# Performance work log

Measured on AMD Instinct MI355X. Metric: run time of the kernel, lower is better.

## Reference

```python
import jax, jax.numpy as jnp
import numpy as np

LN_EPS = 1e-6

def layernorm(x, scale, bias):
    mu = jnp.mean(x, axis=-1, keepdims=True)
    var = jnp.mean(jnp.square(x - mu), axis=-1, keepdims=True)
    return (x - mu) * jax.lax.rsqrt(var + LN_EPS) * scale + bias

def setup_inputs() -> dict:
    key = jax.random.key(0)
    ks = jax.random.split(key, 8)
    B, S, Dm = 2, 2048, 1024
    H, Dh, E, De = 16, 64, 8, 1024
    s = 0.02
    return {
        'x': jax.random.normal(ks[0], (B, S, Dm), jnp.float32),
        'ln1_scale': jnp.ones((Dm,), jnp.float32),
        'ln1_bias': jnp.zeros((Dm,), jnp.float32),
        'Wqkv': jax.random.normal(ks[1], (Dm, 3 * H * Dh), jnp.float32) * s,
        'bqkv': jnp.zeros((3 * H * Dh,), jnp.float32),
        'Wo': jax.random.normal(ks[2], (H * Dh, Dm), jnp.float32) * s,
        'bo': jnp.zeros((Dm,), jnp.float32),
        'ln2_scale': jnp.ones((Dm,), jnp.float32),
        'ln2_bias': jnp.zeros((Dm,), jnp.float32),
        'router_W': jax.random.normal(ks[3], (Dm, E), jnp.float32) * s,
        'We': jax.random.normal(ks[4], (E, Dm, De), jnp.float32) * s,
        'be': jnp.zeros((E, De), jnp.float32),
        'Wmo': jax.random.normal(ks[5], (De, Dm), jnp.float32) * s,
        'bmo': jnp.zeros((Dm,), jnp.float32),
    }

def reference(x, ln1_scale, ln1_bias, Wqkv, bqkv, Wo, bo,
              ln2_scale, ln2_bias, router_W, We, be, Wmo, bmo):
    B, S, Dm = x.shape
    H, Dh = 16, 64
    # ---- attention sublayer ----
    y = layernorm(x, ln1_scale, ln1_bias)
    qkv = (y @ Wqkv + bqkv).reshape(B, S, 3, H, Dh)
    qkv = jnp.transpose(qkv, (2, 0, 3, 1, 4))  # [3,B,H,S,Dh]
    q, k, v = qkv[0], qkv[1], qkv[2]
    scale = 1.0 / jnp.sqrt(jnp.float32(Dh))
    attn = jax.nn.softmax(jnp.einsum('bhsd,bhtd->bhst', q, k) * scale, axis=-1)
    o = jnp.einsum('bhst,bhtd->bhsd', attn, v)
    o = jnp.transpose(o, (0, 2, 1, 3)).reshape(B, S, H * Dh)
    x = x + (o @ Wo + bo)
    # ---- dense soft-MoE sublayer ----
    y = layernorm(x, ln2_scale, ln2_bias)
    routing = jax.nn.softmax(jnp.einsum('bsh,he->bse', y, router_W), axis=-1)
    expert_out = jnp.einsum('bsh,ehf->bsef', y, We) + be  # [B,S,E,De]
    combined = jnp.einsum('bse,bsef->bsf', routing, expert_out)
    x = x + (combined @ Wmo + bmo)
    return x
```

## Files before the change

kernel.cpp:

```cpp
#include <hip/hip_runtime.h>
#include <hip/hip_bf16.h>

typedef unsigned short u16;
typedef float f32x4 __attribute__((ext_vector_type(4)));
typedef short s16x8 __attribute__((ext_vector_type(8)));
typedef unsigned short u16x4 __attribute__((ext_vector_type(4)));
typedef unsigned short u16x8 __attribute__((ext_vector_type(8)));

#define T_TOK 4096
#define DM 1024
#define NQKV 3072
#define LN_EPS 1e-6f
#define KDIM 1024
#define NT 32

__device__ __forceinline__ void gll16(const void* g, void* l) {
    __builtin_amdgcn_global_load_lds(
        (const __attribute__((address_space(1))) void*)g,
        (__attribute__((address_space(3))) void*)l, 16, 0, 0);
}

__device__ __forceinline__ void xcd_swz(int& bx, int& by) {
    const int gx = gridDim.x, gy = gridDim.y;
    const int nwg = gx * gy;
    const int lin = by * gx + bx;
    const int cpx = nwg >> 3;
    const int swz = (lin & 7) * cpx + (lin >> 3);
    bx = swz % gx;
    by = swz / gx;
}

__device__ __forceinline__ void bf16_split(float x, u16& hi, u16& lo) {
    unsigned xb = __float_as_uint(x);
    unsigned rh = xb + 0x7fffu + ((xb >> 16) & 1u);
    hi = (u16)(rh >> 16);
    float hf = __uint_as_float(((unsigned)hi) << 16);
    float rs = x - hf;
    unsigned rb = __float_as_uint(rs);
    unsigned rl = rb + 0x7fffu + ((rb >> 16) & 1u);
    lo = (u16)(rl >> 16);
}
__device__ __forceinline__ u16 f2bf(float x) {
    unsigned xb = __float_as_uint(x);
    return (u16)((xb + 0x7fffu + ((xb >> 16) & 1u)) >> 16);
}
__device__ __forceinline__ float bf16_comb(u16 h, u16 l) {
    return __uint_as_float(((unsigned)h) << 16) + __uint_as_float(((unsigned)l) << 16);
}

#define MFMA3(ACC, AH, AL, BH, BL) { \
    ACC = __builtin_amdgcn_mfma_f32_16x16x32_bf16(AH, BH, ACC, 0, 0, 0); \
    ACC = __builtin_amdgcn_mfma_f32_16x16x32_bf16(AH, BL, ACC, 0, 0, 0); \
    ACC = __builtin_amdgcn_mfma_f32_16x16x32_bf16(AL, BH, ACC, 0, 0, 0); }

__global__ __launch_bounds__(256)
void convert_w(const float* __restrict__ src, u16* __restrict__ dh,
               u16* __restrict__ dl, int K, int N) {
    const int e = blockIdx.z;
    src += (size_t)e * K * N;
    dh  += (size_t)e * K * N;
    dl  += (size_t)e * K * N;
    __shared__ float ts[64][65];
    const int t = threadIdx.x;
    const int k0 = blockIdx.y * 64, n0 = blockIdx.x * 64;
    const int r = t >> 4, c4 = (t & 15) * 4;
    #pragma unroll
    for (int i = 0; i < 4; ++i) {
        const int kr = r + i * 16;
        float4 v = *(const float4*)(src + (size_t)(k0 + kr) * N + n0 + c4);
        ts[kr][c4 + 0] = v.x; ts[kr][c4 + 1] = v.y;
        ts[kr][c4 + 2] = v.z; ts[kr][c4 + 3] = v.w;
    }
    __syncthreads();
    #pragma unroll
    for (int i = 0; i < 4; ++i) {
        const int nr = r + i * 16;
        u16x4 h4, l4;
        #pragma unroll
        for (int j = 0; j < 4; ++j) {
            u16 h, l; bf16_split(ts[c4 + j][nr], h, l);
            h4[j] = h; l4[j] = l;
        }
        *(u16x4*)(dh + (size_t)(n0 + nr) * K + k0 + c4) = h4;
        *(u16x4*)(dl + (size_t)(n0 + nr) * K + k0 + c4) = l4;
    }
}

__global__ __launch_bounds__(256)
void ln_kernel(const float* __restrict__ x, const float* __restrict__ sc,
               const float* __restrict__ bi, u16* __restrict__ yh,
               u16* __restrict__ yl) {
    const int row = blockIdx.x;
    const int t = threadIdx.x;
    const float* xr = x + (size_t)row * DM;
    float4 v = *(const float4*)(xr + t * 4);
    float s  = v.x + v.y + v.z + v.w;
    float s2 = v.x*v.x + v.y*v.y + v.z*v.z + v.w*v.w;
    #pragma unroll
    for (int off = 32; off; off >>= 1) {
        s  += __shfl_down(s, off);
        s2 += __shfl_down(s2, off);
    }
    __shared__ float ss[4], ss2[4];
    const int wid = t >> 6;
    if ((t & 63) == 0) { ss[wid] = s; ss2[wid] = s2; }
    __syncthreads();
    const float tot  = ss[0] + ss[1] + ss[2] + ss[3];
    const float tot2 = ss2[0] + ss2[1] + ss2[2] + ss2[3];
    const float mu  = tot * (1.0f / DM);
    const float var = tot2 * (1.0f / DM) - mu * mu;
    const float rcp = rsqrtf(var + LN_EPS);
    float4 sv = *(const float4*)(sc + t * 4);
    float4 bv = *(const float4*)(bi + t * 4);
    float o[4];
    o[0] = (v.x - mu) * rcp * sv.x + bv.x;
    o[1] = (v.y - mu) * rcp * sv.y + bv.y;
    o[2] = (v.z - mu) * rcp * sv.z + bv.z;
    o[3] = (v.w - mu) * rcp * sv.w + bv.w;
    u16x4 h4, l4;
    #pragma unroll
    for (int j = 0; j < 4; ++j) { u16 h, l; bf16_split(o[j], h, l); h4[j] = h; l4[j] = l; }
    *(u16x4*)(yh + (size_t)row * DM + t * 4) = h4;
    *(u16x4*)(yl + (size_t)row * DM + t * 4) = l4;
}

__global__ __launch_bounds__(256, 2)
void qkv_gemm(const u16* __restrict__ Ah, const u16* __restrict__ Al,
              const u16* __restrict__ Bh, const u16* __restrict__ Bl,
              const float* __restrict__ bias,
              u16* __restrict__ qh, u16* __restrict__ ql,
              u16* __restrict__ kh, u16* __restrict__ kl,
              u16* __restrict__ vh, u16* __restrict__ vl) {
    __shared__ __align__(16) u16 Ahs[128 * 32], Als[128 * 32];
    __shared__ __align__(16) u16 Bhs[128 * 32], Bls[128 * 32];
    int bx = blockIdx.x, by = blockIdx.y;
    xcd_swz(bx, by);
    const int t = threadIdx.x;
    const int m0 = by * 128, n0 = bx * 128;
    const int lane = t & 63, wid = t >> 6;
    const int wm = wid >> 1, wn = wid & 1;
    const int lr = lane & 15, lc = lane >> 4;
    const int srow = lane >> 2, skk = (lane & 3) * 8;
    const int w32 = wid * 32;
    const u16* Agh = Ah + (size_t)(m0 + w32 + srow) * KDIM + skk;
    const u16* Agl = Al + (size_t)(m0 + w32 + srow) * KDIM + skk;
    const u16* Bgh = Bh + (size_t)(n0 + w32 + srow) * KDIM + skk;
    const u16* Bgl = Bl + (size_t)(n0 + w32 + srow) * KDIM + skk;

    f32x4 acc[4][4];
    #pragma unroll
    for (int i = 0; i < 4; ++i)
        #pragma unroll
        for (int j = 0; j < 4; ++j)
            #pragma unroll
            for (int r = 0; r < 4; ++r) acc[i][j][r] = 0.0f;

    for (int kt = 0; kt < NT; ++kt) {
        const int ko = kt * 32;
        gll16(Agh + ko,              &Ahs[w32 * 32]);
        gll16(Agh + ko + 16 * KDIM,  &Ahs[(w32 + 16) * 32]);
        gll16(Agl + ko,              &Als[w32 * 32]);
        gll16(Agl + ko + 16 * KDIM,  &Als[(w32 + 16) * 32]);
        gll16(Bgh + ko,              &Bhs[w32 * 32]);
        gll16(Bgh + ko + 16 * KDIM,  &Bhs[(w32 + 16) * 32]);
        gll16(Bgl + ko,              &Bls[w32 * 32]);
        gll16(Bgl + ko + 16 * KDIM,  &Bls[(w32 + 16) * 32]);
        __syncthreads();
        s16x8 fa_h[4], fa_l[4], fb_h[4], fb_l[4];
        #pragma unroll
        for (int fi = 0; fi < 4; ++fi) {
            const int ro = (wm * 64 + fi * 16 + lr) * 32 + lc * 8;
            fa_h[fi] = *(const s16x8*)&Ahs[ro];
            fa_l[fi] = *(const s16x8*)&Als[ro];
        }
        #pragma unroll
        for (int fj = 0; fj < 4; ++fj) {
            const int ro = (wn * 64 + fj * 16 + lr) * 32 + lc * 8;
            fb_h[fj] = *(const s16x8*)&Bhs[ro];
            fb_l[fj] = *(const s16x8*)&Bls[ro];
        }
        #pragma unroll
        for (int fi = 0; fi < 4; ++fi)
            #pragma unroll
            for (int fj = 0; fj < 4; ++fj)
                MFMA3(acc[fi][fj], fa_h[fi], fa_l[fi], fb_h[fj], fb_l[fj])
        __syncthreads();
    }

    #pragma unroll
    for (int fj = 0; fj < 4; ++fj) {
        const int col = n0 + wn * 64 + fj * 16 + lr;
        const int sec = col >> 10;
        const int hh = (col & 1023) >> 6;
        const int dd = col & 63;
        const float bv = bias[col];
        u16* ph = (sec == 0) ? qh : (sec == 1) ? kh : vh;
        u16* pl = (sec == 0) ? ql : (sec == 1) ? kl : vl;
        #pragma unroll
        for (int fi = 0; fi < 4; ++fi)
            #pragma unroll
            for (int r = 0; r < 4; ++r) {
                const int row = m0 + wm * 64 + fi * 16 + lc * 4 + r;
                const int b = row >> 11, s = row & 2047;
                const size_t idx = ((size_t)(b * 16 + hh) * 2048 + s) * 64 + dd;
                u16 h, l; bf16_split(acc[fi][fj][r] + bv, h, l);
                ph[idx] = h; pl[idx] = l;
            }
    }
}

template<int MODE>
__global__ __launch_bounds__(256, 2)
void gemm_mfma(const u16* __restrict__ Ah, const u16* __restrict__ Al,
               const u16* __restrict__ Bh, const u16* __restrict__ Bl,
               const float* __restrict__ bias, const float* __restrict__ res,
               float* __restrict__ C, u16* __restrict__ Cb, int N) {
    __shared__ __align__(16) u16 Ahs[128 * 32], Als[128 * 32];
    __shared__ __align__(16) u16 Bhs[128 * 32], Bls[128 * 32];
    int bx = blockIdx.x, by = blockIdx.y;
    xcd_swz(bx, by);
    const int t = threadIdx.x;
    const int m0 = by * 128, n0 = bx * 128;
    const int lane = t & 63, wid = t >> 6;
    const int wm = wid >> 1, wn = wid & 1;
    const int lr = lane & 15, lc = lane >> 4;
    const int srow = lane >> 2, skk = (lane & 3) * 8;
    const int w32 = wid * 32;
    const u16* Agh = Ah + (size_t)(m0 + w32 + srow) * KDIM + skk;
    const u16* Agl = Al + (size_t)(m0 + w32 + srow) * KDIM + skk;
    const u16* Bgh = Bh + (size_t)(n0 + w32 + srow) * KDIM + skk;
    const u16* Bgl = Bl + (size_t)(n0 + w32 + srow) * KDIM + skk;

    f32x4 acc[4][4];
    #pragma unroll
    for (int i = 0; i < 4; ++i)
        #pragma unroll
        for (int j = 0; j < 4; ++j)
            #pragma unroll
            for (int r = 0; r < 4; ++r) acc[i][j][r] = 0.0f;

    for (int kt = 0; kt < NT; ++kt) {
        const int ko = kt * 32;
        gll16(Agh + ko,              &Ahs[w32 * 32]);
        gll16(Agh + ko + 16 * KDIM,  &Ahs[(w32 + 16) * 32]);
        gll16(Agl + ko,              &Als[w32 * 32]);
        gll16(Agl + ko + 16 * KDIM,  &Als[(w32 + 16) * 32]);
        gll16(Bgh + ko,              &Bhs[w32 * 32]);
        gll16(Bgh + ko + 16 * KDIM,  &Bhs[(w32 + 16) * 32]);
        gll16(Bgl + ko,              &Bls[w32 * 32]);
        gll16(Bgl + ko + 16 * KDIM,  &Bls[(w32 + 16) * 32]);
        __syncthreads();
        s16x8 fa_h[4], fa_l[4], fb_h[4], fb_l[4];
        #pragma unroll
        for (int fi = 0; fi < 4; ++fi) {
            const int ro = (wm * 64 + fi * 16 + lr) * 32 + lc * 8;
            fa_h[fi] = *(const s16x8*)&Ahs[ro];
            fa_l[fi] = *(const s16x8*)&Als[ro];
        }
        #pragma unroll
        for (int fj = 0; fj < 4; ++fj) {
            const int ro = (wn * 64 + fj * 16 + lr) * 32 + lc * 8;
            fb_h[fj] = *(const s16x8*)&Bhs[ro];
            fb_l[fj] = *(const s16x8*)&Bls[ro];
        }
        #pragma unroll
        for (int fi = 0; fi < 4; ++fi)
            #pragma unroll
            for (int fj = 0; fj < 4; ++fj)
                MFMA3(acc[fi][fj], fa_h[fi], fa_l[fi], fb_h[fj], fb_l[fj])
        __syncthreads();
    }

    #pragma unroll
    for (int fj = 0; fj < 4; ++fj) {
        const int col = n0 + wn * 64 + fj * 16 + lr;
        const float bv = bias[col];
        #pragma unroll
        for (int fi = 0; fi < 4; ++fi)
            #pragma unroll
            for (int r = 0; r < 4; ++r) {
                const int row = m0 + wm * 64 + fi * 16 + lc * 4 + r;
                if (MODE == 0) {
                    C[(size_t)row * N + col] =
                        acc[fi][fj][r] + bv + res[(size_t)row * N + col];
                } else {
                    Cb[(size_t)row * N + col] = f2bf(acc[fi][fj][r] + bv);
                }
            }
    }
}

__global__ __launch_bounds__(256)
void combine_kernel(const u16* __restrict__ eo, const float* __restrict__ r,
                    u16* __restrict__ ch, u16* __restrict__ cl) {
    const int t = blockIdx.x;
    const int f0 = threadIdx.x * 4;
    const float* rt = r + (size_t)t * 8;
    float rr[8];
    #pragma unroll
    for (int e = 0; e < 8; ++e) rr[e] = rt[e];
    const u16* row = eo + (size_t)t * 8192;
    float acc[4] = {0.0f, 0.0f, 0.0f, 0.0f};
    #pragma unroll
    for (int e = 0; e < 8; ++e) {
        u16x4 v = *(const u16x4*)(row + e * 1024 + f0);
        #pragma unroll
        for (int j = 0; j < 4; ++j)
            acc[j] += rr[e] * __uint_as_float(((unsigned)v[j]) << 16);
    }
    u16x4 h4, l4;
    #pragma unroll
    for (int j = 0; j < 4; ++j) { u16 h, l; bf16_split(acc[j], h, l); h4[j] = h; l4[j] = l; }
    *(u16x4*)(ch + (size_t)t * 1024 + f0) = h4;
    *(u16x4*)(cl + (size_t)t * 1024 + f0) = l4;
}

#define VTS 72
__global__ __launch_bounds__(256, 3)
void attn_kernel(const u16* __restrict__ qh, const u16* __restrict__ ql,
                 const u16* __restrict__ kh, const u16* __restrict__ kl,
                 const u16* __restrict__ vh, const u16* __restrict__ vl,
                 u16* __restrict__ oh, u16* __restrict__ ol) {
    __shared__ __align__(16) u16 Khs[64 * 64], Kls[64 * 64];
    __shared__ __align__(16) u16 Vth[64 * VTS], Vtl[64 * VTS];
    __shared__ __align__(16) u16 Phs[4 * 16 * VTS], Pls[4 * 16 * VTS];
    const int t = threadIdx.x;
    const int lane = t & 63, w = t >> 6;
    const int lr = lane & 15, lc = lane >> 4;
    const int q0 = blockIdx.x * 64;
    const int bh = blockIdx.y;
    const int b = bh >> 4, h = bh & 15;
    const size_t head = (size_t)bh * 2048 * 64;

    s16x8 qf_h[2], qf_l[2];
    {
        const size_t qrow = head + (size_t)(q0 + w * 16 + lr) * 64;
        #pragma unroll
        for (int c = 0; c < 2; ++c) {
            qf_h[c] = *(const s16x8*)(qh + qrow + c * 32 + lc * 8);
            qf_l[c] = *(const s16x8*)(ql + qrow + c * 32 + lc * 8);
        }
    }

    f32x4 o4[4];
    #pragma unroll
    for (int dt = 0; dt < 4; ++dt)
        #pragma unroll
        for (int r = 0; r < 4; ++r) o4[dt][r] = 0.0f;
    float m_run[4], l_run[4];
    #pragma unroll
    for (int r = 0; r < 4; ++r) { m_run[r] = -3.0e38f; l_run[r] = 0.0f; }

    char* const kbase_h = (char*)Khs;
    char* const kbase_l = (char*)Kls;
    u16* const pmy_h = Phs + w * 16 * VTS;
    u16* const pmy_l = Pls + w * 16 * VTS;

    const int dbase = (w & 1) * 32;
    const u16* kplane = (w >> 1) ? kl : kh;
    const u16* vplane = (w >> 1) ? vl : vh;
    char* const kdst = (w >> 1) ? kbase_l : kbase_h;
    u16* const vdst = (w >> 1) ? Vtl : Vth;

    u16x8 kreg[4], vreg[4];
    {
        const size_t grow = head + (size_t)(0 * 64 + lane) * 64 + dbase;
        #pragma unroll
        for (int jj = 0; jj < 4; ++jj) {
            kreg[jj] = *(const u16x8*)(kplane + grow + jj * 8);
            vreg[jj] = *(const u16x8*)(vplane + grow + jj * 8);
        }
    }

    for (int kt = 0; kt < 32; ++kt) {
        __syncthreads();
        #pragma unroll
        for (int jj = 0; jj < 4; ++jj) {
            const int off = (lane * 128 + dbase * 2 + jj * 16) ^ ((lane & 7) << 4);
            *(u16x8*)(kdst + off) = kreg[jj];
            #pragma unroll
            for (int i = 0; i < 8; ++i)
                vdst[(dbase + jj * 8 + i) * VTS + lane] = vreg[jj][i];
        }
        if (kt + 1 < 32) {
            const size_t grow = head + (size_t)((kt + 1) * 64 + lane) * 64 + dbase;
            #pragma unroll
            for (int jj = 0; jj < 4; ++jj) {
                kreg[jj] = *(const u16x8*)(kplane + grow + jj * 8);
                vreg[jj] = *(const u16x8*)(vplane + grow + jj * 8);
            }
        }
        __syncthreads();

        f32x4 s4[4];
        const int kxor = (lr & 7) << 4;
        #pragma unroll
        for (int j = 0; j < 4; ++j) {
            #pragma unroll
            for (int r = 0; r < 4; ++r) s4[j][r] = 0.0f;
            #pragma unroll
            for (int c = 0; c < 2; ++c) {
                const int off = ((j * 16 + lr) * 128 + c * 64 + lc * 16) ^ kxor;
                s16x8 kb_h = *(const s16x8*)(kbase_h + off);
                s16x8 kb_l = *(const s16x8*)(kbase_l + off);
                MFMA3(s4[j], qf_h[c], qf_l[c], kb_h, kb_l)
            }
        }
        #pragma unroll
        for (int j = 0; j < 4; ++j)
            #pragma unroll
            for (int r = 0; r < 4; ++r) s4[j][r] *= 0.125f;
        #pragma unroll
        for (int r = 0; r < 4; ++r) {
            float tm = fmaxf(fmaxf(s4[0][r], s4[1][r]), fmaxf(s4[2][r], s4[3][r]));
            tm = fmaxf(tm, __shfl_xor(tm, 1));
            tm = fmaxf(tm, __shfl_xor(tm, 2));
            tm = fmaxf(tm, __shfl_xor(tm, 4));
            tm = fmaxf(tm, __shfl_xor(tm, 8));
            const float mn = fmaxf(m_run[r], tm);
            const float corr = __expf(m_run[r] - mn);
            m_run[r] = mn;
            float ps = 0.0f;
            #pragma unroll
            for (int j = 0; j < 4; ++j) {
                const float p = __expf(s4[j][r] - mn);
                s4[j][r] = p;
                ps += p;
            }
            ps += __shfl_xor(ps, 1);
            ps += __shfl_xor(ps, 2);
            ps += __shfl_xor(ps, 4);
            ps += __shfl_xor(ps, 8);
            l_run[r] = l_run[r] * corr + ps;
            #pragma unroll
            for (int dt = 0; dt < 4; ++dt) o4[dt][r] *= corr;
        }
        #pragma unroll
        for (int j = 0; j < 4; ++j)
            #pragma unroll
            for (int r = 0; r < 4; ++r) {
                u16 ph, pl; bf16_split(s4[j][r], ph, pl);
                const int pidx = (lc * 4 + r) * VTS + j * 16 + lr;
                pmy_h[pidx] = ph;
                pmy_l[pidx] = pl;
            }
        #pragma unroll
        for (int kc = 0; kc < 2; ++kc) {
            const int pbase = lr * VTS + kc * 32 + lc * 8;
            s16x8 pa_h = *(const s16x8*)(pmy_h + pbase);
            s16x8 pa_l = *(const s16x8*)(pmy_l + pbase);
            #pragma unroll
            for (int dt = 0; dt < 4; ++dt) {
                const int vbase = (dt * 16 + lr) * VTS + kc * 32 + lc * 8;
                s16x8 vb_h = *(const s16x8*)(Vth + vbase);
                s16x8 vb_l = *(const s16x8*)(Vtl + vbase);
                MFMA3(o4[dt], pa_h, pa_l, vb_h, vb_l)
            }
        }
    }

    float inv[4];
    #pragma unroll
    for (int r = 0; r < 4; ++r) inv[r] = 1.0f / l_run[r];
    #pragma unroll
    for (int dt = 0; dt < 4; ++dt)
        #pragma unroll
        for (int r = 0; r < 4; ++r) {
            const int tok = b * 2048 + q0 + w * 16 + lc * 4 + r;
            const size_t idx = (size_t)tok * 1024 + h * 64 + dt * 16 + lr;
            u16 hh, ll; bf16_split(o4[dt][r] * inv[r], hh, ll);
            oh[idx] = hh; ol[idx] = ll;
        }
}

__global__ __launch_bounds__(64)
void router_kernel(const u16* __restrict__ yh, const u16* __restrict__ yl,
                   const float* __restrict__ rw, float* __restrict__ r) {
    const int tok = blockIdx.x;
    const int lane = threadIdx.x;
    const u16* yhr = yh + (size_t)tok * DM;
    const u16* ylr = yl + (size_t)tok * DM;
    float acc[8] = {0, 0, 0, 0, 0, 0, 0, 0};
    #pragma unroll
    for (int i = 0; i < 16; ++i) {
        const int hh = i * 64 + lane;
        const float yv = bf16_comb(yhr[hh], ylr[hh]);
        const float4 w0 = *(const float4*)(rw + hh * 8);
        const float4 w1 = *(const float4*)(rw + hh * 8 + 4);
        acc[0] = fmaf(yv, w0.x, acc[0]); acc[1] = fmaf(yv, w0.y, acc[1]);
        acc[2] = fmaf(yv, w0.z, acc[2]); acc[3] = fmaf(yv, w0.w, acc[3]);
        acc[4] = fmaf(yv, w1.x, acc[4]); acc[5] = fmaf(yv, w1.y, acc[5]);
        acc[6] = fmaf(yv, w1.z, acc[6]); acc[7] = fmaf(yv, w1.w, acc[7]);
    }
    #pragma unroll
    for (int off = 32; off; off >>= 1)
        #pragma unroll
        for (int e = 0; e < 8; ++e) acc[e] += __shfl_down(acc[e], off);
    if (lane == 0) {
        float mx = acc[0];
        #pragma unroll
        for (int e = 1; e < 8; ++e) mx = fmaxf(mx, acc[e]);
        float p[8], sum = 0.0f;
        #pragma unroll
        for (int e = 0; e < 8; ++e) { p[e] = __expf(acc[e] - mx); sum += p[e]; }
        const float inv = 1.0f / sum;
        #pragma unroll
        for (int e = 0; e < 8; ++e) r[(size_t)tok * 8 + e] = p[e] * inv;
    }
}

extern "C" void kernel_launch(void* const* d_in, const int* in_sizes, int n_in,
                              void* d_out, int out_size, void* d_ws, size_t ws_size,
                              hipStream_t stream) {
    const float* x    = (const float*)d_in[0];
    const float* ln1s = (const float*)d_in[1];
    const float* ln1b = (const float*)d_in[2];
    const float* Wqkv = (const float*)d_in[3];
    const float* bqkv = (const float*)d_in[4];
    const float* Wo   = (const float*)d_in[5];
    const float* bo   = (const float*)d_in[6];
    const float* ln2s = (const float*)d_in[7];
    const float* ln2b = (const float*)d_in[8];
    const float* rW   = (const float*)d_in[9];
    const float* We   = (const float*)d_in[10];
    const float* be   = (const float*)d_in[11];
    const float* Wmo  = (const float*)d_in[12];
    const float* bmo  = (const float*)d_in[13];
    float* out = (float*)d_out;

    char* w = (char*)d_ws;
    auto carve = [&](size_t bytes) {
        void* p = (void*)w;
        w += (bytes + 255) & ~(size_t)255;
        return p;
    };
    const size_t PL = (size_t)T_TOK * DM;
    u16* qh = (u16*)carve(PL * 2); u16* ql = (u16*)carve(PL * 2);
    u16* kh = (u16*)carve(PL * 2); u16* kl = (u16*)carve(PL * 2);
    u16* vh = (u16*)carve(PL * 2); u16* vl = (u16*)carve(PL * 2);
    u16* ob_h = (u16*)carve(PL * 2); u16* ob_l = (u16*)carve(PL * 2);
    float* x1  = (float*)carve(PL * 4);
    u16* y_h  = (u16*)carve(PL * 2); u16* y_l  = (u16*)carve(PL * 2);
    float* r  = (float*)carve((size_t)T_TOK * 8 * 4);
    u16* Wqkv_h = (u16*)carve((size_t)DM * NQKV * 2);
    u16* Wqkv_l = (u16*)carve((size_t)DM * NQKV * 2);
    u16* Wo_h   = (u16*)carve((size_t)DM * DM * 2);
    u16* Wo_l   = (u16*)carve((size_t)DM * DM * 2);
    u16* We_h   = (u16*)carve((size_t)8 * DM * DM * 2);
    u16* We_l   = (u16*)carve((size_t)8 * DM * DM * 2);
    u16* Wmo_h  = (u16*)carve((size_t)DM * DM * 2);
    u16* Wmo_l  = (u16*)carve((size_t)DM * DM * 2);
    u16* eo = qh;
    u16* cb_h = y_h;
    u16* cb_l = y_l;

    convert_w<<<dim3(NQKV / 64, DM / 64, 1), 256, 0, stream>>>(Wqkv, Wqkv_h, Wqkv_l, DM, NQKV);
    convert_w<<<dim3(DM / 64, DM / 64, 1), 256, 0, stream>>>(Wo, Wo_h, Wo_l, DM, DM);
    convert_w<<<dim3(DM / 64, DM / 64, 8), 256, 0, stream>>>(We, We_h, We_l, DM, DM);
    convert_w<<<dim3(DM / 64, DM / 64, 1), 256, 0, stream>>>(Wmo, Wmo_h, Wmo_l, DM, DM);

    ln_kernel<<<T_TOK, 256, 0, stream>>>(x, ln1s, ln1b, y_h, y_l);
    qkv_gemm<<<dim3(NQKV / 128, T_TOK / 128), 256, 0, stream>>>(
        y_h, y_l, Wqkv_h, Wqkv_l, bqkv, qh, ql, kh, kl, vh, vl);
    attn_kernel<<<dim3(32, 32), 256, 0, stream>>>(qh, ql, kh, kl, vh, vl, ob_h, ob_l);
    gemm_mfma<0><<<dim3(DM / 128, T_TOK / 128), 256, 0, stream>>>(
        ob_h, ob_l, Wo_h, Wo_l, bo, x, x1, nullptr, DM);
    ln_kernel<<<T_TOK, 256, 0, stream>>>(x1, ln2s, ln2b, y_h, y_l);
    router_kernel<<<T_TOK, 64, 0, stream>>>(y_h, y_l, rW, r);
    gemm_mfma<1><<<dim3(8192 / 128, T_TOK / 128), 256, 0, stream>>>(
        y_h, y_l, We_h, We_l, be, nullptr, nullptr, eo, 8192);
    combine_kernel<<<T_TOK, 256, 0, stream>>>(eo, r, cb_h, cb_l);
    gemm_mfma<0><<<dim3(DM / 128, T_TOK / 128), 256, 0, stream>>>(
        cb_h, cb_l, Wmo_h, Wmo_l, bmo, x1, out, nullptr, DM);
}
```

Before: 824.7 us.

## Deepen GEMM K-tile with swizzled LDS, add lazy softmax rescale and MFMA priority

```diff
diff --git a/kernel.cpp b/kernel.cpp
--- a/kernel.cpp
+++ b/kernel.cpp
@@ -13,6 +13,7 @@
 #define LN_EPS 1e-6f
 #define KDIM 1024
 #define NT 32
+#define NT2 16
 
 __device__ __forceinline__ void gll16(const void* g, void* l) {
     __builtin_amdgcn_global_load_lds(
@@ -215,8 +216,8 @@
                const u16* __restrict__ Bh, const u16* __restrict__ Bl,
                const float* __restrict__ bias, const float* __restrict__ res,
                float* __restrict__ C, u16* __restrict__ Cb, int N) {
-    __shared__ __align__(16) u16 Ahs[128 * 32], Als[128 * 32];
-    __shared__ __align__(16) u16 Bhs[128 * 32], Bls[128 * 32];
+    __shared__ __align__(16) u16 Ahs[128 * 64], Als[128 * 64];
+    __shared__ __align__(16) u16 Bhs[128 * 64], Bls[128 * 64];
     int bx = blockIdx.x, by = blockIdx.y;
     xcd_swz(bx, by);
     const int t = threadIdx.x;
@@ -224,7 +225,8 @@
     const int lane = t & 63, wid = t >> 6;
     const int wm = wid >> 1, wn = wid & 1;
     const int lr = lane & 15, lc = lane >> 4;
-    const int srow = lane >> 2, skk = (lane & 3) * 8;
+    const int srow = lane >> 3;
+    const int skk  = ((lane & 7) ^ (lane >> 3)) * 8;
     const int w32 = wid * 32;
     const u16* Agh = Ah + (size_t)(m0 + w32 + srow) * KDIM + skk;
     const u16* Agl = Al + (size_t)(m0 + w32 + srow) * KDIM + skk;
@@ -239,35 +241,40 @@
             #pragma unroll
             for (int r = 0; r < 4; ++r) acc[i][j][r] = 0.0f;
 
-    for (int kt = 0; kt < NT; ++kt) {
-        const int ko = kt * 32;
-        gll16(Agh + ko,              &Ahs[w32 * 32]);
-        gll16(Agh + ko + 16 * KDIM,  &Ahs[(w32 + 16) * 32]);
-        gll16(Agl + ko,              &Als[w32 * 32]);
-        gll16(Agl + ko + 16 * KDIM,  &Als[(w32 + 16) * 32]);
-        gll16(Bgh + ko,              &Bhs[w32 * 32]);
-        gll16(Bgh + ko + 16 * KDIM,  &Bhs[(w32 + 16) * 32]);
-        gll16(Bgl + ko,              &Bls[w32 * 32]);
-        gll16(Bgl + ko + 16 * KDIM,  &Bls[(w32 + 16) * 32]);
+    for (int kt = 0; kt < NT2; ++kt) {
+        const int ko = kt * 64;
+        #pragma unroll
+        for (int i = 0; i < 4; ++i) {
+            const int go = ko + i * 8 * KDIM;
+            gll16(Agh + go, &Ahs[(w32 + i * 8) * 64]);
+            gll16(Agl + go, &Als[(w32 + i * 8) * 64]);
+            gll16(Bgh + go, &Bhs[(w32 + i * 8) * 64]);
+            gll16(Bgl + go, &Bls[(w32 + i * 8) * 64]);
+        }
         __syncthreads();
-        s16x8 fa_h[4], fa_l[4], fb_h[4], fb_l[4];
-        #pragma unroll
-        for (int fi = 0; fi < 4; ++fi) {
-            const int ro = (wm * 64 + fi * 16 + lr) * 32 + lc * 8;
-            fa_h[fi] = *(const s16x8*)&Ahs[ro];
-            fa_l[fi] = *(const s16x8*)&Als[ro];
-        }
-        #pragma unroll
-        for (int fj = 0; fj < 4; ++fj) {
-            const int ro = (wn * 64 + fj * 16 + lr) * 32 + lc * 8;
-            fb_h[fj] = *(const s16x8*)&Bhs[ro];
-            fb_l[fj] = *(const s16x8*)&Bls[ro];
-        }
-        #pragma unroll
-        for (int fi = 0; fi < 4; ++fi)
-            #pragma unroll
-            for (int fj = 0; fj < 4; ++fj)
-                MFMA3(acc[fi][fj], fa_h[fi], fa_l[fi], fb_h[fj], fb_l[fj])
+        #pragma unroll
+        for (int ks = 0; ks < 2; ++ks) {
+            s16x8 fa_h[4], fa_l[4], fb_h[4], fb_l[4];
+            #pragma unroll
+            for (int fi = 0; fi < 4; ++fi) {
+                const int row = wm * 64 + fi * 16 + lr;
+                const int ro = row * 64 + (((ks * 4 + lc) ^ (row & 7)) << 3);
+                fa_h[fi] = *(const s16x8*)&Ahs[ro];
+                fa_l[fi] = *(const s16x8*)&Als[ro];
+            }
+            #pragma unroll
+            for (int fj = 0; fj < 4; ++fj) {
+                const int row = wn * 64 + fj * 16 + lr;
+                const int ro = row * 64 + (((ks * 4 + lc) ^ (row & 7)) << 3);
+                fb_h[fj] = *(const s16x8*)&Bhs[ro];
+                fb_l[fj] = *(const s16x8*)&Bls[ro];
+            }
+            #pragma unroll
+            for (int fi = 0; fi < 4; ++fi)
+                #pragma unroll
+                for (int fj = 0; fj < 4; ++fj)
+                    MFMA3(acc[fi][fj], fa_h[fi], fa_l[fi], fb_h[fj], fb_l[fj])
+        }
         __syncthreads();
     }
 
@@ -394,6 +401,7 @@
 
         f32x4 s4[4];
         const int kxor = (lr & 7) << 4;
+        __builtin_amdgcn_s_setprio(1);
         #pragma unroll
         for (int j = 0; j < 4; ++j) {
             #pragma unroll
@@ -406,10 +414,13 @@
                 MFMA3(s4[j], qf_h[c], qf_l[c], kb_h, kb_l)
             }
         }
+        __builtin_amdgcn_s_setprio(0);
+
         #pragma unroll
         for (int j = 0; j < 4; ++j)
             #pragma unroll
             for (int r = 0; r < 4; ++r) s4[j][r] *= 0.125f;
+        float tmx[4];
         #pragma unroll
         for (int r = 0; r < 4; ++r) {
             float tm = fmaxf(fmaxf(s4[0][r], s4[1][r]), fmaxf(s4[2][r], s4[3][r]));
@@ -417,13 +428,27 @@
             tm = fmaxf(tm, __shfl_xor(tm, 2));
             tm = fmaxf(tm, __shfl_xor(tm, 4));
             tm = fmaxf(tm, __shfl_xor(tm, 8));
-            const float mn = fmaxf(m_run[r], tm);
-            const float corr = __expf(m_run[r] - mn);
-            m_run[r] = mn;
+            tmx[r] = tm;
+        }
+        const bool grow_m = (tmx[0] > m_run[0] + 8.0f) || (tmx[1] > m_run[1] + 8.0f) ||
+                            (tmx[2] > m_run[2] + 8.0f) || (tmx[3] > m_run[3] + 8.0f);
+        if (__any(grow_m)) {
+            #pragma unroll
+            for (int r = 0; r < 4; ++r) {
+                const float mn = fmaxf(m_run[r], tmx[r]);
+                const float corr = __expf(m_run[r] - mn);
+                m_run[r] = mn;
+                l_run[r] *= corr;
+                #pragma unroll
+                for (int dt = 0; dt < 4; ++dt) o4[dt][r] *= corr;
+            }
+        }
+        #pragma unroll
+        for (int r = 0; r < 4; ++r) {
             float ps = 0.0f;
             #pragma unroll
             for (int j = 0; j < 4; ++j) {
-                const float p = __expf(s4[j][r] - mn);
+                const float p = __expf(s4[j][r] - m_run[r]);
                 s4[j][r] = p;
                 ps += p;
             }
@@ -431,9 +456,7 @@
             ps += __shfl_xor(ps, 2);
             ps += __shfl_xor(ps, 4);
             ps += __shfl_xor(ps, 8);
-            l_run[r] = l_run[r] * corr + ps;
-            #pragma unroll
-            for (int dt = 0; dt < 4; ++dt) o4[dt][r] *= corr;
+            l_run[r] += ps;
         }
         #pragma unroll
         for (int j = 0; j < 4; ++j)
@@ -444,6 +467,7 @@
                 pmy_h[pidx] = ph;
                 pmy_l[pidx] = pl;
             }
+        __builtin_amdgcn_s_setprio(1);
         #pragma unroll
         for (int kc = 0; kc < 2; ++kc) {
             const int pbase = lr * VTS + kc * 32 + lc * 8;
@@ -457,6 +481,7 @@
                 MFMA3(o4[dt], pa_h, pa_l, vb_h, vb_l)
             }
         }
+        __builtin_amdgcn_s_setprio(0);
     }
 
     float inv[4];
```

After: 764.0 us. 7.4% less time.
